# Kernel optimization log

Measured on AMD Instinct MI355X. Metric: run time of the kernel, lower is better.

The kernel has to match this reference:

```python
import jax, jax.numpy as jnp
import numpy as np

RADIUS = 0.2
NSAMPLE = 32
NPOINT = 2048
EPS = 1e-5


def setup_inputs() -> dict:
    key = jax.random.key(0)
    ks = jax.random.split(key, 6)
    B, N, C = 8, 8192, 64
    xyz = jax.random.uniform(ks[0], (B, N, 3), dtype=jnp.float32)
    features = jax.random.normal(ks[1], (B, C, N), dtype=jnp.float32)
    W1 = jax.random.normal(ks[2], (64, 67), dtype=jnp.float32) * 0.1
    W2 = jax.random.normal(ks[3], (64, 64), dtype=jnp.float32) * 0.1
    W3 = jax.random.normal(ks[4], (128, 64), dtype=jnp.float32) * 0.1
    return {
        'xyz': xyz, 'features': features,
        'W1': W1, 'g1': jnp.ones((64,), jnp.float32), 'b1': jnp.zeros((64,), jnp.float32),
        'W2': W2, 'g2': jnp.ones((64,), jnp.float32), 'b2': jnp.zeros((64,), jnp.float32),
        'W3': W3, 'g3': jnp.ones((128,), jnp.float32), 'b3': jnp.zeros((128,), jnp.float32),
    }


def furthest_point_sample(xyz, npoint):
    # xyz: (B, N, 3) -> (B, npoint) int32 indices, first index is 0 (CUDA FPS convention)
    B, N, _ = xyz.shape
    idxs0 = jnp.zeros((B, npoint), dtype=jnp.int32)
    dists0 = jnp.full((B, N), 1e10, dtype=xyz.dtype)
    last0 = jnp.zeros((B,), dtype=jnp.int32)

    def body(i, state):
        idxs, dists, last = state
        last_pt = xyz[jnp.arange(B), last]                      # (B, 3)
        d = jnp.sum((xyz - last_pt[:, None, :]) ** 2, axis=-1)  # (B, N)
        dists = jnp.minimum(dists, d)
        nxt = jnp.argmax(dists, axis=-1).astype(jnp.int32)
        idxs = idxs.at[:, i].set(nxt)
        return (idxs, dists, nxt)

    idxs, _, _ = jax.lax.fori_loop(1, npoint, body, (idxs0, dists0, last0))
    return idxs


def ball_query(xyz, new_xyz, radius, nsample):
    # Returns (B, S, nsample) int32: first `nsample` points within radius of each
    # query center, padded with the first in-ball index (pointnet2 convention).
    N = xyz.shape[1]
    d2 = jnp.sum((new_xyz[:, :, None, :] - xyz[:, None, :, :]) ** 2, axis=-1)  # (B,S,N)
    key = jnp.where(d2 < radius * radius, jnp.arange(N, dtype=jnp.int32), N)
    neg_vals, _ = jax.lax.top_k(-key, nsample)   # k smallest keys = earliest in-ball indices
    cand = -neg_vals                             # (B, S, nsample)
    first = cand[..., :1]
    return jnp.where(cand < N, cand, first)


def reference(xyz, features, W1, g1, b1, W2, g2, b2, W3, g3, b3):
    B = xyz.shape[0]
    fps_idx = furthest_point_sample(xyz, NPOINT)              # (B, S)
    new_xyz = xyz[jnp.arange(B)[:, None], fps_idx]            # (B, S, 3)

    idx = ball_query(xyz, new_xyz, RADIUS, NSAMPLE)           # (B, S, ns)
    bb = jnp.arange(B)[:, None, None]
    grouped_xyz = xyz[bb, idx] - new_xyz[:, :, None, :]       # (B, S, ns, 3) relative coords
    grouped_f = features.transpose(0, 2, 1)[bb, idx]          # (B, S, ns, C)
    g = jnp.concatenate([grouped_xyz, grouped_f], axis=-1)    # (B, S, ns, 3+C)
    g = g.transpose(0, 3, 1, 2)                               # (B, 3+C, S, ns)

    for W, ga, be in ((W1, g1, b1), (W2, g2, b2), (W3, g3, b3)):
        h = jnp.einsum('oc,bcsn->bosn', W, g)                 # 1x1 conv
        mu = h.mean(axis=(0, 2, 3), keepdims=True)            # training-mode BN stats
        var = h.var(axis=(0, 2, 3), keepdims=True)
        h = (h - mu) / jnp.sqrt(var + EPS)
        g = jax.nn.relu(h * ga[None, :, None, None] + be[None, :, None, None])

    feats = g.max(axis=-1)                                    # (B, mlp[-1], S)
    return new_xyz, feats
```

## Files before the change

### kernel.cpp

```cpp
#include <hip/hip_runtime.h>
#include <hip/hip_bf16.h>
#include <stdint.h>

#define NB 8
#define NN 8192
#define NC 64
#define NS 2048
#define NK 32
#define NCOL (NB*NS*NK)

typedef float v2f __attribute__((ext_vector_type(2)));
typedef __attribute__((ext_vector_type(8))) short bf16x8;
typedef __attribute__((ext_vector_type(4))) float f32x4;

__device__ __forceinline__ unsigned short f2bf(float x) {
    union { float f; unsigned u; } c; c.f = x;
    unsigned r = c.u + 0x7fffu + ((c.u >> 16) & 1u);
    return (unsigned short)(r >> 16);
}
__device__ __forceinline__ float bf2f(unsigned v16) {
    union { float f; unsigned u; } c; c.u = v16 << 16;
    return c.f;
}

template<int CTRL>
__device__ __forceinline__ unsigned long long dpp_max_u64(unsigned long long key) {
    int olo = __builtin_amdgcn_update_dpp(0, (int)(unsigned)key,        CTRL, 0xf, 0xf, true);
    int ohi = __builtin_amdgcn_update_dpp(0, (int)(unsigned)(key >> 32), CTRL, 0xf, 0xf, true);
    unsigned long long ok = ((unsigned long long)(unsigned)ohi << 32) | (unsigned)olo;
    return ok > key ? ok : key;
}
template<int CTRL>
__device__ __forceinline__ float dpp_add_f32(float x) {
    int o = __builtin_amdgcn_update_dpp(0, __float_as_int(x), CTRL, 0xf, 0xf, true);
    return x + __int_as_float(o);
}
template<int CTRL>
__device__ __forceinline__ float dpp_max_f32(float x) {
    int o = __builtin_amdgcn_update_dpp(__float_as_int(x), __float_as_int(x), CTRL, 0xf, 0xf, false);
    return fmaxf(x, __int_as_float(o));
}
template<int CTRL>
__device__ __forceinline__ float dpp_min_f32(float x) {
    int o = __builtin_amdgcn_update_dpp(__float_as_int(x), __float_as_int(x), CTRL, 0xf, 0xf, false);
    return fminf(x, __int_as_float(o));
}
template<int CTRL, int RM>
__device__ __forceinline__ unsigned dpp_add_u32(unsigned x) {
    int o = __builtin_amdgcn_update_dpp(0, (int)x, CTRL, RM, 0xf, true);
    return x + (unsigned)o;
}
__device__ __forceinline__ float wave_red_min(float x) {
    x = dpp_min_f32<0x111>(x); x = dpp_min_f32<0x112>(x);
    x = dpp_min_f32<0x114>(x); x = dpp_min_f32<0x118>(x);
    x = dpp_min_f32<0x142>(x); x = dpp_min_f32<0x143>(x);
    return __int_as_float(__builtin_amdgcn_readlane(__float_as_int(x), 63));
}
__device__ __forceinline__ float wave_red_max(float x) {
    x = dpp_max_f32<0x111>(x); x = dpp_max_f32<0x112>(x);
    x = dpp_max_f32<0x114>(x); x = dpp_max_f32<0x118>(x);
    x = dpp_max_f32<0x142>(x); x = dpp_max_f32<0x143>(x);
    return __int_as_float(__builtin_amdgcn_readlane(__float_as_int(x), 63));
}
__device__ __forceinline__ v2f relu2(v2f v) {
    v.x = fmaxf(v.x, 0.f); v.y = fmaxf(v.y, 0.f); return v;
}

__device__ __forceinline__ unsigned expand_bits10(unsigned v) {
    v = (v * 0x00010001u) & 0xFF0000FFu;
    v = (v * 0x00000101u) & 0x0F00F00Fu;
    v = (v * 0x00000011u) & 0xC30C30C3u;
    v = (v * 0x00000005u) & 0x49249249u;
    return v;
}
__global__ __launch_bounds__(1024) void sort_kernel(const float* __restrict__ xyz,
    float4* __restrict__ sorted)
{
    __shared__ unsigned cnt[2048];
    __shared__ unsigned codes[NN];
    __shared__ unsigned wsum[16];
    const int b = blockIdx.x;
    const int tid = threadIdx.x;
    const int w = tid >> 6;
    const int lane = tid & 63;
    const float* xb = xyz + (size_t)b * NN * 3;
    cnt[tid] = 0; cnt[tid + 1024] = 0;
    __syncthreads();
    for (int p = tid; p < NN; p += 1024) {
        float x = xb[3*p+0], y = xb[3*p+1], z = xb[3*p+2];
        int qx = (int)(x * 1024.f); qx = qx < 0 ? 0 : (qx > 1023 ? 1023 : qx);
        int qy = (int)(y * 1024.f); qy = qy < 0 ? 0 : (qy > 1023 ? 1023 : qy);
        int qz = (int)(z * 1024.f); qz = qz < 0 ? 0 : (qz > 1023 ? 1023 : qz);
        unsigned m = expand_bits10((unsigned)qx)
                   | (expand_bits10((unsigned)qy) << 1)
                   | (expand_bits10((unsigned)qz) << 2);
        unsigned bk = m >> 19;
        codes[p] = bk;
        atomicAdd(&cnt[bk], 1u);
    }
    __syncthreads();
    unsigned c0 = cnt[2*tid], c1 = cnt[2*tid+1];
    unsigned s = c0 + c1;
    unsigned v = s;
    v = dpp_add_u32<0x111, 0xf>(v);
    v = dpp_add_u32<0x112, 0xf>(v);
    v = dpp_add_u32<0x114, 0xf>(v);
    v = dpp_add_u32<0x118, 0xf>(v);
    v = dpp_add_u32<0x142, 0xa>(v);
    v = dpp_add_u32<0x143, 0xc>(v);
    if (lane == 63) wsum[w] = v;
    __syncthreads();
    unsigned wbase = 0;
#pragma unroll
    for (int j = 0; j < 15; ++j) {
        unsigned t = wsum[j];
        wbase += (j < w) ? t : 0u;
    }
    unsigned excl = wbase + v - s;
    cnt[2*tid]   = excl;
    cnt[2*tid+1] = excl + c0;
    __syncthreads();
    for (int p = tid; p < NN; p += 1024) {
        unsigned bk = codes[p];
        unsigned pos = atomicAdd(&cnt[bk], 1u);
        float4 o;
        o.x = xb[3*p+0]; o.y = xb[3*p+1]; o.z = xb[3*p+2];
        o.w = __int_as_float(p);
        sorted[(size_t)b * NN + pos] = o;
    }
}

__global__ __launch_bounds__(1024) void fps_kernel(const float* __restrict__ xyz,
    const float4* __restrict__ sorted,
    float* __restrict__ new_xyz, float* __restrict__ out_newxyz)
{
#pragma clang fp contract(off)
    const int b = blockIdx.x;
    const int tid = threadIdx.x;
    const int w = tid >> 6;
    const int lane = tid & 63;
    __shared__ float sx[NN], sy[NN], sz[NN];
    __shared__ float s_hist[NS * 3];
    __shared__ unsigned long long s_slot[3];
    const float4* sp = sorted + (size_t)b * NN + (size_t)w * 512 + lane;
    v2f px[4], py[4], pz[4], dmin[4];
    unsigned plo[8];
    float bnx = 1e30f, bny = 1e30f, bnz = 1e30f;
    float bxx = -1e30f, bxy = -1e30f, bxz = -1e30f;
#pragma unroll
    for (int m = 0; m < 4; ++m) {
        float4 a = sp[128*m];
        float4 c = sp[128*m + 64];
        px[m].x = a.x; px[m].y = c.x;
        py[m].x = a.y; py[m].y = c.y;
        pz[m].x = a.z; pz[m].y = c.z;
        dmin[m].x = 1e10f; dmin[m].y = 1e10f;
        int ia = __float_as_int(a.w), ic = __float_as_int(c.w);
        plo[2*m]   = ~(unsigned)ia;
        plo[2*m+1] = ~(unsigned)ic;
        sx[ia] = a.x; sy[ia] = a.y; sz[ia] = a.z;
        sx[ic] = c.x; sy[ic] = c.y; sz[ic] = c.z;
        bnx = fminf(bnx, fminf(a.x, c.x)); bxx = fmaxf(bxx, fmaxf(a.x, c.x));
        bny = fminf(bny, fminf(a.y, c.y)); bxy = fmaxf(bxy, fmaxf(a.y, c.y));
        bnz = fminf(bnz, fminf(a.z, c.z)); bxz = fmaxf(bxz, fmaxf(a.z, c.z));
    }
    bnx = wave_red_min(bnx); bny = wave_red_min(bny); bnz = wave_red_min(bnz);
    bxx = wave_red_max(bxx); bxy = wave_red_max(bxy); bxz = wave_red_max(bxz);

    const float* xb = xyz + (size_t)b * NN * 3;
    float lx = xb[0], ly = xb[1], lz = xb[2];
    if (tid == 0) {
        s_hist[0] = lx; s_hist[1] = ly; s_hist[2] = lz;
        s_slot[0] = 0ull; s_slot[1] = 0ull; s_slot[2] = 0ull;
    }
    float ckv = 1e30f;
    unsigned cklo = 0u;
    __syncthreads();

    int cur = 1, nxt = 2;
    for (int i = 1; i < NS; ++i) {
        if (tid == 0) s_slot[nxt] = 0ull;
        float cdx = fmaxf(fmaxf(bnx - lx, lx - bxx), 0.f);
        float cdy = fmaxf(fmaxf(bny - ly, ly - bxy), 0.f);
        float cdz = fmaxf(fmaxf(bnz - lz, lz - bxz), 0.f);
        float lb = (cdx*cdx + cdy*cdy) + cdz*cdz;
        if (!(lb >= ckv)) {
            v2f l2x; l2x.x = lx; l2x.y = lx;
            v2f l2y; l2y.x = ly; l2y.y = ly;
            v2f l2z; l2z.x = lz; l2z.y = lz;
            unsigned long long best = 0ull;
#pragma unroll
            for (int m = 0; m < 4; ++m) {
                v2f dx = px[m] - l2x;
                v2f dy = py[m] - l2y;
                v2f dz = pz[m] - l2z;
                v2f d = (dx*dx + dy*dy) + dz*dz;
                v2f dm;
                dm.x = fminf(dmin[m].x, d.x);
                dm.y = fminf(dmin[m].y, d.y);
                dmin[m] = dm;
                unsigned long long k0 =
                    ((unsigned long long)__float_as_uint(dm.x) << 32) | plo[2*m];
                unsigned long long k1 =
                    ((unsigned long long)__float_as_uint(dm.y) << 32) | plo[2*m+1];
                if (k0 > best) best = k0;
                if (k1 > best) best = k1;
            }
            best = dpp_max_u64<0x111>(best);
            best = dpp_max_u64<0x112>(best);
            best = dpp_max_u64<0x114>(best);
            best = dpp_max_u64<0x118>(best);
            best = dpp_max_u64<0x142>(best);
            best = dpp_max_u64<0x143>(best);
            ckv  = __uint_as_float((unsigned)__builtin_amdgcn_readlane((int)(best >> 32), 63));
            cklo = (unsigned)__builtin_amdgcn_readlane((int)(best & 0xffffffffull), 63);
        }
        if (lane == 0)
            atomicMax(&s_slot[cur],
                      ((unsigned long long)__float_as_uint(ckv) << 32) | cklo);
        __syncthreads();
        const unsigned long long k = s_slot[cur];
        const int ix = ~(int)(unsigned)(k & 0xffffffffull);
        lx = sx[ix]; ly = sy[ix]; lz = sz[ix];
        if (tid == 0) {
            s_hist[3*i+0] = lx; s_hist[3*i+1] = ly; s_hist[3*i+2] = lz;
        }
        cur = nxt;
        nxt = nxt + 1; if (nxt == 3) nxt = 0;
    }
    __syncthreads();
    float* nw = new_xyz + (size_t)b * NS * 3;
    float* ow = out_newxyz + (size_t)b * NS * 3;
    for (int t = tid; t < NS * 3; t += 1024) {
        float v = s_hist[t];
        nw[t] = v; ow[t] = v;
    }
}

__global__ __launch_bounds__(256) void transpose_kernel(const float* __restrict__ f,
    float* __restrict__ ft)
{
    __shared__ float tile[64][65];
    int b = blockIdx.y;
    int p0 = blockIdx.x * 64;
    for (int k = threadIdx.x; k < 64*64; k += 256) {
        int c = k >> 6, p = k & 63;
        tile[c][p] = f[((size_t)b * NC + c) * NN + p0 + p];
    }
    __syncthreads();
    for (int k = threadIdx.x; k < 64*64; k += 256) {
        int p = k >> 6, c = k & 63;
        ft[((size_t)b * NN + p0 + p) * NC + c] = tile[c][p];
    }
}

__global__ __launch_bounds__(256) void ballquery_kernel(const float* __restrict__ xyz,
    const float* __restrict__ new_xyz, int* __restrict__ idx)
{
#pragma clang fp contract(off)
    const int q = blockIdx.x * 4 + (threadIdx.x >> 6);
    const int lane = threadIdx.x & 63;
    const int b = q >> 11;
    const float r2 = (float)(0.2 * 0.2);
    const float* xb = xyz + (size_t)b * NN * 3;
    const float* nx = new_xyz + (size_t)q * 3;
    float qx = nx[0], qy = nx[1], qz = nx[2];
    int cnt = 0, first = -1;
    int* out = idx + (size_t)q * NK;
    for (int base = 0; base < NN; base += 64) {
        int p = base + lane;
        float x = xb[p*3+0], y = xb[p*3+1], z = xb[p*3+2];
        float dx = qx - x, dy = qy - y, dz = qz - z;
        float d2 = (dx*dx + dy*dy) + dz*dz;
        bool in = d2 < r2;
        unsigned long long m = __ballot(in);
        if (m) {
            if (first < 0) first = base + __builtin_ctzll(m);
            if (in) {
                int rank = cnt + __popcll(m & ((1ull << lane) - 1ull));
                if (rank < NK) out[rank] = p;
            }
            cnt += __popcll(m);
            if (cnt >= NK) break;
        }
    }
    for (int k = cnt + lane; k < NK; k += 64) out[k] = first;
}

__global__ __launch_bounds__(256, 2) void layer1_kernel(const float* __restrict__ xyz,
    const float* __restrict__ new_xyz, const int* __restrict__ idx,
    const float* __restrict__ ft, const float* __restrict__ W1,
    unsigned short* __restrict__ h1)
{
    const int col = blockIdx.x * 256 + threadIdx.x;
    const int b = col >> 16;
    const int s = (col >> 5) & 2047;
    const int p = idx[col];
    v2f g[34];
    float* gf = (float*)g;
    {
        const float* nx = new_xyz + ((size_t)(b * NS + s)) * 3;
        const float* xp = xyz + ((size_t)(b * NN + p)) * 3;
        gf[0] = xp[0] - nx[0]; gf[1] = xp[1] - nx[1]; gf[2] = xp[2] - nx[2];
    }
    const float4* fp = (const float4*)(ft + ((size_t)(b * NN + p)) * NC);
#pragma unroll
    for (int c4 = 0; c4 < 16; ++c4) {
        float4 v = fp[c4];
        gf[3 + 4*c4 + 0] = v.x; gf[3 + 4*c4 + 1] = v.y;
        gf[3 + 4*c4 + 2] = v.z; gf[3 + 4*c4 + 3] = v.w;
    }
    gf[67] = 0.f;
    uint4* dst = (uint4*)(h1 + (size_t)col * 64);
#pragma unroll
    for (int half = 0; half < 2; ++half) {
        float h[32];
#pragma unroll 4
        for (int o16 = 0; o16 < 32; ++o16) {
            const float* w = W1 + (half*32 + o16) * 67;
            v2f acc; acc.x = 0.f; acc.y = 0.f;
#pragma unroll
            for (int k = 0; k < 33; ++k) {
                v2f wv; wv.x = w[2*k]; wv.y = w[2*k+1];
                acc = wv * g[k] + acc;
            }
            h[o16] = fmaf(w[66], gf[66], acc.x + acc.y);
        }
#pragma unroll
        for (int k = 0; k < 4; ++k) {
            uint4 v;
            v.x = (unsigned)f2bf(h[8*k+0]) | ((unsigned)f2bf(h[8*k+1]) << 16);
            v.y = (unsigned)f2bf(h[8*k+2]) | ((unsigned)f2bf(h[8*k+3]) << 16);
            v.z = (unsigned)f2bf(h[8*k+4]) | ((unsigned)f2bf(h[8*k+5]) << 16);
            v.w = (unsigned)f2bf(h[8*k+6]) | ((unsigned)f2bf(h[8*k+7]) << 16);
            dst[half*4 + k] = v;
        }
    }
}

__global__ __launch_bounds__(256) void stats_kernel(const unsigned short* __restrict__ h,
    float* __restrict__ sums)
{
    __shared__ float ls[64], lq[64];
    const int tid = threadIdx.x;
    if (tid < 64) { ls[tid] = 0.f; lq[tid] = 0.f; }
    __syncthreads();
    float s[8] = {0,0,0,0,0,0,0,0}, q[8] = {0,0,0,0,0,0,0,0};
    const int gt = blockIdx.x * 256 + tid;
    const int G = gridDim.x * 256;
    const uint4* src = (const uint4*)h;
    const int nvec = NCOL * 8;
    for (int i = gt; i < nvec; i += G) {
        uint4 v = src[i];
        float f0 = bf2f(v.x & 0xffffu), f1 = bf2f(v.x >> 16);
        float f2 = bf2f(v.y & 0xffffu), f3 = bf2f(v.y >> 16);
        float f4 = bf2f(v.z & 0xffffu), f5 = bf2f(v.z >> 16);
        float f6 = bf2f(v.w & 0xffffu), f7 = bf2f(v.w >> 16);
        s[0] += f0; q[0] = fmaf(f0, f0, q[0]);
        s[1] += f1; q[1] = fmaf(f1, f1, q[1]);
        s[2] += f2; q[2] = fmaf(f2, f2, q[2]);
        s[3] += f3; q[3] = fmaf(f3, f3, q[3]);
        s[4] += f4; q[4] = fmaf(f4, f4, q[4]);
        s[5] += f5; q[5] = fmaf(f5, f5, q[5]);
        s[6] += f6; q[6] = fmaf(f6, f6, q[6]);
        s[7] += f7; q[7] = fmaf(f7, f7, q[7]);
    }
    const int obase = (tid & 7) * 8;
#pragma unroll
    for (int j = 0; j < 8; ++j) {
        atomicAdd(&ls[obase + j], s[j]);
        atomicAdd(&lq[obase + j], q[j]);
    }
    __syncthreads();
    if (tid < 64) {
        atomicAdd(&sums[tid*2+0], ls[tid]);
        atomicAdd(&sums[tid*2+1], lq[tid]);
    }
}

__global__ void finalize_kernel(const float* __restrict__ sums,
    const float* __restrict__ gamma, const float* __restrict__ beta,
    float* __restrict__ ab, int nch)
{
    int c = threadIdx.x;
    if (c < nch) {
        const float invM = 1.0f / 524288.0f;
        float mu = sums[c*2] * invM;
        float var = sums[c*2+1] * invM - mu * mu;
        float a = gamma[c] / sqrtf(var + 1e-5f);
        ab[c] = a;
        ab[nch + c] = fmaf(-mu, a, beta[c]);
    }
}

__global__ __launch_bounds__(256, 2) void layer2_kernel(const unsigned short* __restrict__ h1,
    const float* __restrict__ ab1, const float* __restrict__ W2,
    unsigned short* __restrict__ h2)
{
    const int tid = threadIdx.x;
    const int lane = tid & 63;
    const int col0 = lane & 15;
    const int rg   = lane >> 4;
    const int wglob = blockIdx.x * 4 + (tid >> 6);

    for (int g = wglob * 2; g < wglob * 2 + 2; ++g) {
        bf16x8 Bf[2][2];
#pragma unroll
        for (int t = 0; t < 2; ++t) {
            const int col = g * 32 + t * 16 + col0;
            const unsigned short* hp = h1 + (size_t)col * 64 + rg * 8;
#pragma unroll
            for (int kh = 0; kh < 2; ++kh) {
                uint4 hv = *(const uint4*)(hp + kh * 32);
                const float* ap = ab1 + kh * 32 + rg * 8;
                float4 a0 = *(const float4*)ap;
                float4 a1 = *(const float4*)(ap + 4);
                float4 b0 = *(const float4*)(ap + 64);
                float4 b1 = *(const float4*)(ap + 68);
                bf16x8 f;
                f[0] = (short)f2bf(fmaxf(fmaf(a0.x, bf2f(hv.x & 0xffffu), b0.x), 0.f));
                f[1] = (short)f2bf(fmaxf(fmaf(a0.y, bf2f(hv.x >> 16),     b0.y), 0.f));
                f[2] = (short)f2bf(fmaxf(fmaf(a0.z, bf2f(hv.y & 0xffffu), b0.z), 0.f));
                f[3] = (short)f2bf(fmaxf(fmaf(a0.w, bf2f(hv.y >> 16),     b0.w), 0.f));
                f[4] = (short)f2bf(fmaxf(fmaf(a1.x, bf2f(hv.z & 0xffffu), b1.x), 0.f));
                f[5] = (short)f2bf(fmaxf(fmaf(a1.y, bf2f(hv.z >> 16),     b1.y), 0.f));
                f[6] = (short)f2bf(fmaxf(fmaf(a1.z, bf2f(hv.w & 0xffffu), b1.z), 0.f));
                f[7] = (short)f2bf(fmaxf(fmaf(a1.w, bf2f(hv.w >> 16),     b1.w), 0.f));
                Bf[t][kh] = f;
            }
        }
#pragma unroll
        for (int rt = 0; rt < 4; ++rt) {
            f32x4 acc0 = {0.f, 0.f, 0.f, 0.f};
            f32x4 acc1 = {0.f, 0.f, 0.f, 0.f};
#pragma unroll
            for (int kh = 0; kh < 2; ++kh) {
                const float* wp = W2 + (size_t)(rt * 16 + col0) * 64 + kh * 32 + rg * 8;
                float4 w0 = *(const float4*)wp;
                float4 w1 = *(const float4*)(wp + 4);
                bf16x8 Af;
                Af[0] = (short)f2bf(w0.x); Af[1] = (short)f2bf(w0.y);
                Af[2] = (short)f2bf(w0.z); Af[3] = (short)f2bf(w0.w);
                Af[4] = (short)f2bf(w1.x); Af[5] = (short)f2bf(w1.y);
                Af[6] = (short)f2bf(w1.z); Af[7] = (short)f2bf(w1.w);
                acc0 = __builtin_amdgcn_mfma_f32_16x16x32_bf16(Af, Bf[0][kh], acc0, 0, 0, 0);
                acc1 = __builtin_amdgcn_mfma_f32_16x16x32_bf16(Af, Bf[1][kh], acc1, 0, 0, 0);
            }
            {
                const int col = g * 32 + 0 * 16 + col0;
                uint2 v;
                v.x = (unsigned)f2bf(acc0[0]) | ((unsigned)f2bf(acc0[1]) << 16);
                v.y = (unsigned)f2bf(acc0[2]) | ((unsigned)f2bf(acc0[3]) << 16);
                *(uint2*)(h2 + (size_t)col * 64 + rt * 16 + rg * 4) = v;
            }
            {
                const int col = g * 32 + 1 * 16 + col0;
                uint2 v;
                v.x = (unsigned)f2bf(acc1[0]) | ((unsigned)f2bf(acc1[1]) << 16);
                v.y = (unsigned)f2bf(acc1[2]) | ((unsigned)f2bf(acc1[3]) << 16);
                *(uint2*)(h2 + (size_t)col * 64 + rt * 16 + rg * 4) = v;
            }
        }
    }
}

__global__ __launch_bounds__(256, 2) void layer3_kernel(const unsigned short* __restrict__ h2,
    const float* __restrict__ ab2, const float* __restrict__ W3,
    float* __restrict__ hmax, float* __restrict__ hmin, float* __restrict__ sums3)
{
    __shared__ float ls[128], lq[128];
    const int tid = threadIdx.x;
    if (tid < 128) { ls[tid] = 0.f; lq[tid] = 0.f; }
    __syncthreads();
    const int lane = tid & 63;
    const int col0 = lane & 15;
    const int rg   = lane >> 4;
    const int wglob = blockIdx.x * 4 + (tid >> 6);

    float sums[32], sqs[32];
#pragma unroll
    for (int t = 0; t < 32; ++t) { sums[t] = 0.f; sqs[t] = 0.f; }

    for (int g = wglob * 2; g < wglob * 2 + 2; ++g) {
        bf16x8 Bf[2][2];
#pragma unroll
        for (int t = 0; t < 2; ++t) {
            const int col = g * 32 + t * 16 + col0;
            const unsigned short* hp = h2 + (size_t)col * 64 + rg * 8;
#pragma unroll
            for (int kh = 0; kh < 2; ++kh) {
                uint4 hv = *(const uint4*)(hp + kh * 32);
                const float* ap = ab2 + kh * 32 + rg * 8;
                float4 a0 = *(const float4*)ap;
                float4 a1 = *(const float4*)(ap + 4);
                float4 b0 = *(const float4*)(ap + 64);
                float4 b1 = *(const float4*)(ap + 68);
                bf16x8 f;
                f[0] = (short)f2bf(fmaxf(fmaf(a0.x, bf2f(hv.x & 0xffffu), b0.x), 0.f));
                f[1] = (short)f2bf(fmaxf(fmaf(a0.y, bf2f(hv.x >> 16),     b0.y), 0.f));
                f[2] = (short)f2bf(fmaxf(fmaf(a0.z, bf2f(hv.y & 0xffffu), b0.z), 0.f));
                f[3] = (short)f2bf(fmaxf(fmaf(a0.w, bf2f(hv.y >> 16),     b0.w), 0.f));
                f[4] = (short)f2bf(fmaxf(fmaf(a1.x, bf2f(hv.z & 0xffffu), b1.x), 0.f));
                f[5] = (short)f2bf(fmaxf(fmaf(a1.y, bf2f(hv.z >> 16),     b1.y), 0.f));
                f[6] = (short)f2bf(fmaxf(fmaf(a1.z, bf2f(hv.w & 0xffffu), b1.z), 0.f));
                f[7] = (short)f2bf(fmaxf(fmaf(a1.w, bf2f(hv.w >> 16),     b1.w), 0.f));
                Bf[t][kh] = f;
            }
        }
#pragma unroll
        for (int rt = 0; rt < 8; ++rt) {
            f32x4 acc0 = {0.f, 0.f, 0.f, 0.f};
            f32x4 acc1 = {0.f, 0.f, 0.f, 0.f};
#pragma unroll
            for (int kh = 0; kh < 2; ++kh) {
                const float* wp = W3 + (size_t)(rt * 16 + col0) * 64 + kh * 32 + rg * 8;
                float4 w0 = *(const float4*)wp;
                float4 w1 = *(const float4*)(wp + 4);
                bf16x8 Af;
                Af[0] = (short)f2bf(w0.x); Af[1] = (short)f2bf(w0.y);
                Af[2] = (short)f2bf(w0.z); Af[3] = (short)f2bf(w0.w);
                Af[4] = (short)f2bf(w1.x); Af[5] = (short)f2bf(w1.y);
                Af[6] = (short)f2bf(w1.z); Af[7] = (short)f2bf(w1.w);
                acc0 = __builtin_amdgcn_mfma_f32_16x16x32_bf16(Af, Bf[0][kh], acc0, 0, 0, 0);
                acc1 = __builtin_amdgcn_mfma_f32_16x16x32_bf16(Af, Bf[1][kh], acc1, 0, 0, 0);
            }
#pragma unroll
            for (int r = 0; r < 4; ++r) {
                float v0 = acc0[r], v1 = acc1[r];
                sums[rt*4 + r] += v0 + v1;
                sqs[rt*4 + r]  = fmaf(v0, v0, fmaf(v1, v1, sqs[rt*4 + r]));
                float mx = fmaxf(v0, v1);
                float mn = fminf(v0, v1);
                mx = dpp_max_f32<0x111>(mx); mn = dpp_min_f32<0x111>(mn);
                mx = dpp_max_f32<0x112>(mx); mn = dpp_min_f32<0x112>(mn);
                mx = dpp_max_f32<0x114>(mx); mn = dpp_min_f32<0x114>(mn);
                mx = dpp_max_f32<0x118>(mx); mn = dpp_min_f32<0x118>(mn);
                if (col0 == 15) {
                    const int o = rt * 16 + rg * 4 + r;
                    hmax[(size_t)o * 16384 + g] = mx;
                    hmin[(size_t)o * 16384 + g] = mn;
                }
            }
        }
    }
#pragma unroll
    for (int t = 0; t < 32; ++t) {
        float sm = sums[t], sq = sqs[t];
        sm = dpp_add_f32<0x111>(sm); sq = dpp_add_f32<0x111>(sq);
        sm = dpp_add_f32<0x112>(sm); sq = dpp_add_f32<0x112>(sq);
        sm = dpp_add_f32<0x114>(sm); sq = dpp_add_f32<0x114>(sq);
        sm = dpp_add_f32<0x118>(sm); sq = dpp_add_f32<0x118>(sq);
        if (col0 == 15) {
            const int o = (t >> 2) * 16 + rg * 4 + (t & 3);
            atomicAdd(&ls[o], sm);
            atomicAdd(&lq[o], sq);
        }
    }
    __syncthreads();
    if (tid < 128) {
        atomicAdd(&sums3[tid*2+0], ls[tid]);
        atomicAdd(&sums3[tid*2+1], lq[tid]);
    }
}

__global__ __launch_bounds__(256) void final_kernel(const float* __restrict__ hmax,
    const float* __restrict__ hmin, const float* __restrict__ ab3,
    float* __restrict__ out)
{
    const int t = blockIdx.x * 256 + threadIdx.x;
    const int s = t & 2047;
    const int o = (t >> 11) & 127;
    const int b = t >> 18;
    const int q = (b << 11) + s;
    float a = ab3[o], c = ab3[128 + o];
    float h = (a >= 0.f) ? hmax[(size_t)o * 16384 + q] : hmin[(size_t)o * 16384 + q];
    out[t] = fmaxf(fmaf(a, h, c), 0.f);
}

extern "C" void kernel_launch(void* const* d_in, const int* in_sizes, int n_in,
                              void* d_out, int out_size, void* d_ws, size_t ws_size,
                              hipStream_t stream) {
    (void)in_sizes; (void)n_in; (void)out_size; (void)ws_size;
    const float* xyz      = (const float*)d_in[0];
    const float* features = (const float*)d_in[1];
    const float* W1 = (const float*)d_in[2];
    const float* g1 = (const float*)d_in[3];
    const float* b1 = (const float*)d_in[4];
    const float* W2 = (const float*)d_in[5];
    const float* g2 = (const float*)d_in[6];
    const float* b2 = (const float*)d_in[7];
    const float* W3 = (const float*)d_in[8];
    const float* g3 = (const float*)d_in[9];
    const float* b3 = (const float*)d_in[10];

    char* ws = (char*)d_ws;
    float*          new_xyz = (float*)(ws + 0);
    int*            idx     = (int*)(ws + 196608);
    float*          ft      = (float*)(ws + 2293760);
    unsigned short* h1      = (unsigned short*)(ws + 19070976);
    unsigned short* h2      = (unsigned short*)(ws + 86179840);
    float*          hmax    = (float*)(ws + 153288704);
    float*          hmin    = (float*)(ws + 161677312);
    float*          sums    = (float*)(ws + 170065920);
    float*          ab      = (float*)(ws + 170067968);
    float* sums1 = sums;        float* ab1 = ab;
    float* sums2 = sums + 128;  float* ab2 = ab + 128;
    float* sums3 = sums + 256;  float* ab3 = ab + 256;

    float4* sorted = (float4*)h1;

    float* out_newxyz = (float*)d_out;
    float* out_feats  = (float*)d_out + 49152;

    hipMemsetAsync(sums, 0, 2048, stream);

    sort_kernel<<<NB, 1024, 0, stream>>>(xyz, sorted);
    fps_kernel<<<NB, 1024, 0, stream>>>(xyz, sorted, new_xyz, out_newxyz);
    transpose_kernel<<<dim3(NN/64, NB), 256, 0, stream>>>(features, ft);
    ballquery_kernel<<<(NB*NS)/4, 256, 0, stream>>>(xyz, new_xyz, idx);
    layer1_kernel<<<NCOL/256, 256, 0, stream>>>(xyz, new_xyz, idx, ft, W1, h1);
    stats_kernel<<<1024, 256, 0, stream>>>(h1, sums1);
    finalize_kernel<<<1, 128, 0, stream>>>(sums1, g1, b1, ab1, 64);
    layer2_kernel<<<2048, 256, 0, stream>>>(h1, ab1, W2, h2);
    stats_kernel<<<1024, 256, 0, stream>>>(h2, sums2);
    finalize_kernel<<<1, 128, 0, stream>>>(sums2, g2, b2, ab2, 64);
    layer3_kernel<<<2048, 256, 0, stream>>>(h2, ab2, W3, hmax, hmin, sums3);
    finalize_kernel<<<1, 128, 0, stream>>>(sums3, g3, b3, ab3, 128);
    final_kernel<<<(NB*128*NS)/256, 256, 0, stream>>>(hmax, hmin, ab3, out_feats);
}
```

Baseline: 1.890 ms.

## Fuse feature transpose into FPS launch and layer-2 BN stats into layer2

The feature transpose now runs in extra blocks of the FPS launch, so it can overlap the FPS work, which occupies only 8 blocks and leaves most CUs idle. Layer 2 now accumulates per-channel sum and sum-of-squares of its bf16-rounded outputs using DPP reductions, LDS atomics and then global atomics, which removes a separate stats pass that re-read h2. The cost is extra register pressure in layer2 and a heavier 1024-thread transpose block that competes with FPS for resources.

```diff
diff --git a/kernel.cpp b/kernel.cpp
--- a/kernel.cpp
+++ b/kernel.cpp
@@ -130,18 +130,41 @@
     }
 }
 
-__global__ __launch_bounds__(1024) void fps_kernel(const float* __restrict__ xyz,
+__global__ __launch_bounds__(1024) void fps_tr_kernel(const float* __restrict__ xyz,
     const float4* __restrict__ sorted,
-    float* __restrict__ new_xyz, float* __restrict__ out_newxyz)
+    float* __restrict__ new_xyz, float* __restrict__ out_newxyz,
+    const float* __restrict__ feat, float* __restrict__ ft)
 {
 #pragma clang fp contract(off)
-    const int b = blockIdx.x;
     const int tid = threadIdx.x;
-    const int w = tid >> 6;
-    const int lane = tid & 63;
     __shared__ float sx[NN], sy[NN], sz[NN];
     __shared__ float s_hist[NS * 3];
     __shared__ unsigned long long s_slot[3];
+
+    if (blockIdx.x >= NB) {
+        float* tbuf = sx;
+        const int base = ((int)blockIdx.x - NB) * 4;
+        for (int j = 0; j < 4; ++j) {
+            const int t = base + j;
+            const int b = t >> 7;
+            const int p0 = (t & 127) << 6;
+            for (int k = tid; k < 4096; k += 1024) {
+                int c = k >> 6, p = k & 63;
+                tbuf[c * 65 + p] = feat[((size_t)b * NC + c) * NN + p0 + p];
+            }
+            __syncthreads();
+            for (int k = tid; k < 4096; k += 1024) {
+                int p = k >> 6, c = k & 63;
+                ft[((size_t)b * NN + p0 + p) * NC + c] = tbuf[c * 65 + p];
+            }
+            __syncthreads();
+        }
+        return;
+    }
+
+    const int b = blockIdx.x;
+    const int w = tid >> 6;
+    const int lane = tid & 63;
     const float4* sp = sorted + (size_t)b * NN + (size_t)w * 512 + lane;
     v2f px[4], py[4], pz[4], dmin[4];
     unsigned plo[8];
@@ -234,23 +257,6 @@
     for (int t = tid; t < NS * 3; t += 1024) {
         float v = s_hist[t];
         nw[t] = v; ow[t] = v;
-    }
-}
-
-__global__ __launch_bounds__(256) void transpose_kernel(const float* __restrict__ f,
-    float* __restrict__ ft)
-{
-    __shared__ float tile[64][65];
-    int b = blockIdx.y;
-    int p0 = blockIdx.x * 64;
-    for (int k = threadIdx.x; k < 64*64; k += 256) {
-        int c = k >> 6, p = k & 63;
-        tile[c][p] = f[((size_t)b * NC + c) * NN + p0 + p];
-    }
-    __syncthreads();
-    for (int k = threadIdx.x; k < 64*64; k += 256) {
-        int p = k >> 6, c = k & 63;
-        ft[((size_t)b * NN + p0 + p) * NC + c] = tile[c][p];
     }
 }
 
@@ -395,13 +401,20 @@
 
 __global__ __launch_bounds__(256, 2) void layer2_kernel(const unsigned short* __restrict__ h1,
     const float* __restrict__ ab1, const float* __restrict__ W2,
-    unsigned short* __restrict__ h2)
-{
+    unsigned short* __restrict__ h2, float* __restrict__ sums2)
+{
+    __shared__ float ls[64], lq[64];
     const int tid = threadIdx.x;
+    if (tid < 64) { ls[tid] = 0.f; lq[tid] = 0.f; }
+    __syncthreads();
     const int lane = tid & 63;
     const int col0 = lane & 15;
     const int rg   = lane >> 4;
     const int wglob = blockIdx.x * 4 + (tid >> 6);
+
+    float sums[16], sqs[16];
+#pragma unroll
+    for (int t = 0; t < 16; ++t) { sums[t] = 0.f; sqs[t] = 0.f; }
 
     for (int g = wglob * 2; g < wglob * 2 + 2; ++g) {
         bf16x8 Bf[2][2];
@@ -446,21 +459,46 @@
                 acc0 = __builtin_amdgcn_mfma_f32_16x16x32_bf16(Af, Bf[0][kh], acc0, 0, 0, 0);
                 acc1 = __builtin_amdgcn_mfma_f32_16x16x32_bf16(Af, Bf[1][kh], acc1, 0, 0, 0);
             }
+            unsigned u00 = f2bf(acc0[0]), u01 = f2bf(acc0[1]);
+            unsigned u02 = f2bf(acc0[2]), u03 = f2bf(acc0[3]);
+            unsigned u10 = f2bf(acc1[0]), u11 = f2bf(acc1[1]);
+            unsigned u12 = f2bf(acc1[2]), u13 = f2bf(acc1[3]);
             {
                 const int col = g * 32 + 0 * 16 + col0;
-                uint2 v;
-                v.x = (unsigned)f2bf(acc0[0]) | ((unsigned)f2bf(acc0[1]) << 16);
-                v.y = (unsigned)f2bf(acc0[2]) | ((unsigned)f2bf(acc0[3]) << 16);
+                uint2 v; v.x = u00 | (u01 << 16); v.y = u02 | (u03 << 16);
                 *(uint2*)(h2 + (size_t)col * 64 + rt * 16 + rg * 4) = v;
             }
             {
                 const int col = g * 32 + 1 * 16 + col0;
-                uint2 v;
-                v.x = (unsigned)f2bf(acc1[0]) | ((unsigned)f2bf(acc1[1]) << 16);
-                v.y = (unsigned)f2bf(acc1[2]) | ((unsigned)f2bf(acc1[3]) << 16);
+                uint2 v; v.x = u10 | (u11 << 16); v.y = u12 | (u13 << 16);
                 *(uint2*)(h2 + (size_t)col * 64 + rt * 16 + rg * 4) = v;
             }
-        }
+#pragma unroll
+            for (int r = 0; r < 4; ++r) {
+                float r0 = bf2f(r == 0 ? u00 : r == 1 ? u01 : r == 2 ? u02 : u03);
+                float r1 = bf2f(r == 0 ? u10 : r == 1 ? u11 : r == 2 ? u12 : u13);
+                sums[rt*4 + r] += r0 + r1;
+                sqs[rt*4 + r]  = fmaf(r0, r0, fmaf(r1, r1, sqs[rt*4 + r]));
+            }
+        }
+    }
+#pragma unroll
+    for (int t = 0; t < 16; ++t) {
+        float sm = sums[t], sq = sqs[t];
+        sm = dpp_add_f32<0x111>(sm); sq = dpp_add_f32<0x111>(sq);
+        sm = dpp_add_f32<0x112>(sm); sq = dpp_add_f32<0x112>(sq);
+        sm = dpp_add_f32<0x114>(sm); sq = dpp_add_f32<0x114>(sq);
+        sm = dpp_add_f32<0x118>(sm); sq = dpp_add_f32<0x118>(sq);
+        if (col0 == 15) {
+            const int o = (t >> 2) * 16 + rg * 4 + (t & 3);
+            atomicAdd(&ls[o], sm);
+            atomicAdd(&lq[o], sq);
+        }
+    }
+    __syncthreads();
+    if (tid < 64) {
+        atomicAdd(&sums2[tid*2+0], ls[tid]);
+        atomicAdd(&sums2[tid*2+1], lq[tid]);
     }
 }
 
@@ -615,14 +653,13 @@
     hipMemsetAsync(sums, 0, 2048, stream);
 
     sort_kernel<<<NB, 1024, 0, stream>>>(xyz, sorted);
-    fps_kernel<<<NB, 1024, 0, stream>>>(xyz, sorted, new_xyz, out_newxyz);
-    transpose_kernel<<<dim3(NN/64, NB), 256, 0, stream>>>(features, ft);
+    fps_tr_kernel<<<NB + 256, 1024, 0, stream>>>(xyz, sorted, new_xyz, out_newxyz,
+                                                 features, ft);
     ballquery_kernel<<<(NB*NS)/4, 256, 0, stream>>>(xyz, new_xyz, idx);
     layer1_kernel<<<NCOL/256, 256, 0, stream>>>(xyz, new_xyz, idx, ft, W1, h1);
     stats_kernel<<<1024, 256, 0, stream>>>(h1, sums1);
     finalize_kernel<<<1, 128, 0, stream>>>(sums1, g1, b1, ab1, 64);
-    layer2_kernel<<<2048, 256, 0, stream>>>(h1, ab1, W2, h2);
-    stats_kernel<<<1024, 256, 0, stream>>>(h2, sums2);
+    layer2_kernel<<<2048, 256, 0, stream>>>(h1, ab1, W2, h2, sums2);
     finalize_kernel<<<1, 128, 0, stream>>>(sums2, g2, b2, ab2, 64);
     layer3_kernel<<<2048, 256, 0, stream>>>(h2, ab2, W3, hmax, hmin, sums3);
     finalize_kernel<<<1, 128, 0, stream>>>(sums3, g3, b3, ab3, 128);
```

After: 1.865 ms (median of 2 runs). About the same (-1.3%).
